# Optimization experiments

Measured on AMD Instinct MI355X. Metric: run time of the kernel, lower is better.

Reference implementation:

```python
import jax, jax.numpy as jnp
import numpy as np

N_NODES = 10000
N_EDGES = 160000
IN_FEAT = 1024
H_FEAT = 1024
NUM_CLASSES = 64


def setup_inputs() -> dict:
    key = jax.random.key(0)
    ks = jax.random.split(key, 8)
    h = jax.random.normal(ks[0], (N_NODES, IN_FEAT), dtype=jnp.float32)
    src = jax.random.randint(ks[1], (N_EDGES,), 0, N_NODES, dtype=jnp.int32)
    dst = jax.random.randint(ks[2], (N_EDGES,), 0, N_NODES, dtype=jnp.int32)
    # Xavier-ish scaled weights (DGL uses xavier_uniform for GraphConv)
    W1 = jax.random.normal(ks[3], (IN_FEAT, H_FEAT), dtype=jnp.float32) * (1.0 / np.sqrt(IN_FEAT))
    b1 = jnp.zeros((H_FEAT,), dtype=jnp.float32)
    W2 = jax.random.normal(ks[4], (H_FEAT, H_FEAT), dtype=jnp.float32) * (1.0 / np.sqrt(H_FEAT))
    b2 = jnp.zeros((H_FEAT,), dtype=jnp.float32)
    W3 = jax.random.normal(ks[5], (H_FEAT, NUM_CLASSES), dtype=jnp.float32) * (1.0 / np.sqrt(H_FEAT))
    b3 = jnp.zeros((NUM_CLASSES,), dtype=jnp.float32)
    return {"h": h, "src": src, "dst": dst,
            "W1": W1, "b1": b1, "W2": W2, "b2": b2, "W3": W3, "b3": b3}


def _graph_conv(src, dst, norm_src, norm_dst, x, W, b):
    """DGL GraphConv with norm='both':
    out = D_dst^{-1/2} * sum_{(u,v) in E} (D_src^{-1/2} * x)_u  @ W + b
    """
    xs = x * norm_src[:, None]                     # [N, d] scaled source feats
    msg = xs[src]                                  # [E, d] gather
    agg = jax.ops.segment_sum(msg, dst, num_segments=N_NODES)  # [N, d] scatter-add
    agg = agg * norm_dst[:, None]
    return agg @ W + b


def reference(h, src, dst, W1, b1, W2, b2, W3, b3):
    ones = jnp.ones((N_EDGES,), dtype=jnp.float32)
    deg_out = jax.ops.segment_sum(ones, src, num_segments=N_NODES)  # out-degree of src
    deg_in = jax.ops.segment_sum(ones, dst, num_segments=N_NODES)   # in-degree of dst
    norm_src = jnp.clip(deg_out, 1.0, None) ** -0.5
    norm_dst = jnp.clip(deg_in, 1.0, None) ** -0.5

    x = _graph_conv(src, dst, norm_src, norm_dst, h, W1, b1)
    x = jax.nn.relu(x)
    x = _graph_conv(src, dst, norm_src, norm_dst, x, W2, b2)
    x = jax.nn.relu(x)
    x = _graph_conv(src, dst, norm_src, norm_dst, x, W3, b3)
    return x
```

## Files before the change

kernel.cpp:

```cpp
#include <hip/hip_runtime.h>

constexpr int NN   = 10000;
constexpr int NE   = 160000;
constexpr int F    = 1024;
constexpr int C3   = 64;
constexpr int MPAD = 10112;

typedef __attribute__((ext_vector_type(8))) short short8;
typedef __attribute__((ext_vector_type(8))) unsigned short ushort8v;
typedef __attribute__((ext_vector_type(4))) float floatx4;

__device__ __forceinline__ unsigned short f2bf(float f) {
    union { float f; unsigned u; } v; v.f = f;
    unsigned r = v.u + 0x7fff + ((v.u >> 16) & 1);
    return (unsigned short)(r >> 16);
}
__device__ __forceinline__ float bf2f(unsigned short u) {
    union { unsigned u; float f; } v; v.u = ((unsigned)u) << 16;
    return v.f;
}

__device__ __forceinline__ void gl_lds16(const void* g, void* l) {
    __builtin_amdgcn_global_load_lds(
        (const __attribute__((address_space(1))) unsigned int*)g,
        (__attribute__((address_space(3))) unsigned int*)l, 16, 0, 0);
}


__global__ __launch_bounds__(256) void k_degree(const int* __restrict__ src,
                                                const int* __restrict__ dst,
                                                int* __restrict__ deg_out,
                                                int* __restrict__ deg_in) {
    int e = blockIdx.x * 256 + threadIdx.x;
    if (e < NE) {
        atomicAdd(&deg_out[src[e]], 1);
        atomicAdd(&deg_in[dst[e]], 1);
    }
}

__global__ __launch_bounds__(1024) void k_scan(const int* __restrict__ deg_in,
                                               const int* __restrict__ deg_out,
                                               int* __restrict__ row_ptr,
                                               int* __restrict__ cursor,
                                               float* __restrict__ norm_src,
                                               float* __restrict__ norm_dst) {
    constexpr int CH = 10;
    __shared__ int sums[1024];
    const int tid = threadIdx.x;
    int local[CH];
    int tsum = 0;
#pragma unroll
    for (int j = 0; j < CH; ++j) {
        int idx = tid * CH + j;
        int v = (idx < NN) ? deg_in[idx] : 0;
        local[j] = v;
        tsum += v;
        if (idx < MPAD) {
            norm_src[idx] = rsqrtf(fmaxf((float)deg_out[idx], 1.0f));
            norm_dst[idx] = rsqrtf(fmaxf((float)deg_in[idx], 1.0f));
        }
    }
    sums[tid] = tsum;
    __syncthreads();
    for (int off = 1; off < 1024; off <<= 1) {
        int v = (tid >= off) ? sums[tid - off] : 0;
        __syncthreads();
        sums[tid] += v;
        __syncthreads();
    }
    int run = sums[tid] - tsum;
#pragma unroll
    for (int j = 0; j < CH; ++j) {
        int idx = tid * CH + j;
        if (idx < NN) {
            row_ptr[idx] = run;
            cursor[idx]  = run;
        }
        run += local[j];
    }
    if (tid == 1023) row_ptr[NN] = sums[1023];
}

__global__ __launch_bounds__(256) void k_bucket(const int* __restrict__ src,
                                                const int* __restrict__ dst,
                                                int* __restrict__ cursor,
                                                int* __restrict__ csr_src) {
    int e = blockIdx.x * 256 + threadIdx.x;
    if (e < NE) {
        int slot = atomicAdd(&cursor[dst[e]], 1);
        csr_src[slot] = src[e];
    }
}

__global__ __launch_bounds__(256) void k_wconv_all(const float* __restrict__ W1,
                                                   const float* __restrict__ W2,
                                                   const float* __restrict__ W3,
                                                   unsigned short* __restrict__ Wt1,
                                                   unsigned short* __restrict__ Wt2,
                                                   unsigned short* __restrict__ Wt3) {
    __shared__ float tile[32][33];
    const float* W; unsigned short* Wt; int N, n0, k0;
    int b = blockIdx.x;
    if (b < 1024)      { W = W1; Wt = Wt1; N = F;  n0 = (b & 31) * 32;          k0 = (b >> 5) * 32; }
    else if (b < 2048) { b -= 1024; W = W2; Wt = Wt2; N = F;  n0 = (b & 31) * 32; k0 = (b >> 5) * 32; }
    else               { b -= 2048; W = W3; Wt = Wt3; N = C3; n0 = (b & 1) * 32;  k0 = (b >> 1) * 32; }
    const int tx = threadIdx.x & 31, ty = threadIdx.x >> 5;
#pragma unroll
    for (int i = 0; i < 32; i += 8)
        tile[ty + i][tx] = W[(size_t)(k0 + ty + i) * N + n0 + tx];
    __syncthreads();
#pragma unroll
    for (int i = 0; i < 32; i += 8)
        Wt[(size_t)(n0 + ty + i) * F + k0 + tx] = f2bf(tile[tx][ty + i]);
}


__global__ __launch_bounds__(256) void k_hcvt(const float* __restrict__ h,
                                              const float* __restrict__ norm_src,
                                              unsigned short* __restrict__ hb) {
    int idx = blockIdx.x * 256 + threadIdx.x;
    int v = idx >> 7, f8 = (idx & 127) * 8;
    float ns = norm_src[v];
    const float4 a = *(const float4*)(h + (size_t)v * F + f8);
    const float4 b = *(const float4*)(h + (size_t)v * F + f8 + 4);
    ushort8v o;
    o[0] = f2bf(ns * a.x); o[1] = f2bf(ns * a.y);
    o[2] = f2bf(ns * a.z); o[3] = f2bf(ns * a.w);
    o[4] = f2bf(ns * b.x); o[5] = f2bf(ns * b.y);
    o[6] = f2bf(ns * b.z); o[7] = f2bf(ns * b.w);
    *(ushort8v*)(hb + (size_t)v * F + f8) = o;
}

__global__ __launch_bounds__(256) void k_aggb(const unsigned short* __restrict__ xb,
                                              const int* __restrict__ row_ptr,
                                              const int* __restrict__ csr_src,
                                              unsigned short* __restrict__ aggb) {
    const int c = blockIdx.x & 7;
    const int g = blockIdx.x >> 3;
    const int v = g * 16 + (threadIdx.x >> 4);
    const int f8 = c * 128 + (threadIdx.x & 15) * 8;
    const int lo = row_ptr[v], hi = row_ptr[v + 1];
    float acc[8] = {0.f, 0.f, 0.f, 0.f, 0.f, 0.f, 0.f, 0.f};
    int i = lo;
    for (; i + 4 <= hi; i += 4) {
        int s0 = csr_src[i],     s1 = csr_src[i + 1];
        int s2 = csr_src[i + 2], s3 = csr_src[i + 3];
        ushort8v x0 = *(const ushort8v*)(xb + (size_t)s0 * F + f8);
        ushort8v x1 = *(const ushort8v*)(xb + (size_t)s1 * F + f8);
        ushort8v x2 = *(const ushort8v*)(xb + (size_t)s2 * F + f8);
        ushort8v x3 = *(const ushort8v*)(xb + (size_t)s3 * F + f8);
#pragma unroll
        for (int j = 0; j < 8; ++j) acc[j] += bf2f(x0[j]);
#pragma unroll
        for (int j = 0; j < 8; ++j) acc[j] += bf2f(x1[j]);
#pragma unroll
        for (int j = 0; j < 8; ++j) acc[j] += bf2f(x2[j]);
#pragma unroll
        for (int j = 0; j < 8; ++j) acc[j] += bf2f(x3[j]);
    }
    for (; i < hi; ++i) {
        int s = csr_src[i];
        ushort8v xv = *(const ushort8v*)(xb + (size_t)s * F + f8);
#pragma unroll
        for (int j = 0; j < 8; ++j) acc[j] += bf2f(xv[j]);
    }
    ushort8v o;
#pragma unroll
    for (int j = 0; j < 8; ++j) o[j] = f2bf(acc[j]);
    *(ushort8v*)(aggb + (size_t)v * F + f8) = o;
}

__global__ __launch_bounds__(256) void k_agg64(const float* __restrict__ z,
                                               const int* __restrict__ row_ptr,
                                               const int* __restrict__ csr_src,
                                               const float* __restrict__ norm_dst,
                                               const float* __restrict__ b3,
                                               float* __restrict__ out) {
    const int v = blockIdx.x * 16 + (threadIdx.x >> 4);
    if (v >= NN) return;
    const int f4 = (threadIdx.x & 15) * 4;
    const int lo = row_ptr[v], hi = row_ptr[v + 1];
    float4 acc = {0.f, 0.f, 0.f, 0.f};
    int i = lo;
    for (; i + 2 <= hi; i += 2) {
        int s0 = csr_src[i], s1 = csr_src[i + 1];
        float4 z0 = *(const float4*)(z + (size_t)s0 * C3 + f4);
        float4 z1 = *(const float4*)(z + (size_t)s1 * C3 + f4);
        acc.x += z0.x; acc.y += z0.y; acc.z += z0.z; acc.w += z0.w;
        acc.x += z1.x; acc.y += z1.y; acc.z += z1.z; acc.w += z1.w;
    }
    if (i < hi) {
        int s = csr_src[i];
        float4 zv = *(const float4*)(z + (size_t)s * C3 + f4);
        acc.x += zv.x; acc.y += zv.y; acc.z += zv.z; acc.w += zv.w;
    }
    float nd = norm_dst[v];
    float4 bv = *(const float4*)(b3 + f4);
    float4 o;
    o.x = acc.x * nd + bv.x; o.y = acc.y * nd + bv.y;
    o.z = acc.z * nd + bv.z; o.w = acc.w * nd + bv.w;
    *(float4*)(out + (size_t)v * C3 + f4) = o;
}

__global__ __launch_bounds__(512) void k_gemm_bf16(
        const unsigned short* __restrict__ A,
        const unsigned short* __restrict__ Bt,
        const float* __restrict__ bias,
        const float* __restrict__ rs1,
        const float* __restrict__ rs2,
        unsigned short* __restrict__ Cb) {
    __shared__ short As[2][128 * 32];
    __shared__ short Bs[2][128 * 32];
    const int t = threadIdx.x, lane = t & 63, wid = t >> 6;
    const int m0 = blockIdx.x * 128, n0 = blockIdx.y * 128;
    const int wm0 = (wid & 1) * 64, wn0 = (wid >> 1) * 32;
    const int lr = lane & 15, q = lane >> 4;

    const int rS  = wid * 16 + (lane >> 2);
    const int sS  = (((lane & 3) ^ ((rS >> 1) & 3)) * 8);
    const unsigned short* aSrc = A  + (size_t)(m0 + rS) * F + sS;
    const unsigned short* bSrc = Bt + (size_t)(n0 + rS) * F + sS;
    short* aDst = &As[0][wid * 512];
    short* bDst = &Bs[0][wid * 512];

    const short* ap[4];
    const short* bp[2];
#pragma unroll
    for (int mb = 0; mb < 4; ++mb) {
        int m = wm0 + mb * 16 + lr;
        ap[mb] = &As[0][m * 32 + (q ^ ((m >> 1) & 3)) * 8];
    }
#pragma unroll
    for (int nb = 0; nb < 2; ++nb) {
        int n = wn0 + nb * 16 + lr;
        bp[nb] = &Bs[0][n * 32 + (q ^ ((n >> 1) & 3)) * 8];
    }

    floatx4 acc[4][2] = {};

    gl_lds16(aSrc, aDst);
    gl_lds16(bSrc, bDst);

    for (int kt = 0; kt < F / 32; ++kt) {
        const int buf = kt & 1;
        __syncthreads();
        if (kt + 1 < F / 32) {
            int k0 = (kt + 1) * 32;
            gl_lds16(aSrc + k0, aDst + (buf ^ 1) * (128 * 32));
            gl_lds16(bSrc + k0, bDst + (buf ^ 1) * (128 * 32));
        }
        const int bo = buf * (128 * 32);
        short8 af[4], bf[2];
#pragma unroll
        for (int mb = 0; mb < 4; ++mb) af[mb] = *(const short8*)(ap[mb] + bo);
#pragma unroll
        for (int nb = 0; nb < 2; ++nb) bf[nb] = *(const short8*)(bp[nb] + bo);
#pragma unroll
        for (int mb = 0; mb < 4; ++mb)
#pragma unroll
            for (int nb = 0; nb < 2; ++nb)
                acc[mb][nb] = __builtin_amdgcn_mfma_f32_16x16x32_bf16(
                    af[mb], bf[nb], acc[mb][nb], 0, 0, 0);
    }

    float s1[4][4], s2[4][4];
#pragma unroll
    for (int mb = 0; mb < 4; ++mb)
#pragma unroll
        for (int r = 0; r < 4; ++r) {
            int row = m0 + wm0 + mb * 16 + q * 4 + r;
            s1[mb][r] = rs1[row];
            s2[mb][r] = rs2[row];
        }
#pragma unroll
    for (int nb = 0; nb < 2; ++nb) {
        int col = n0 + wn0 + nb * 16 + lr;
        float bv = bias[col];
#pragma unroll
        for (int mb = 0; mb < 4; ++mb)
#pragma unroll
            for (int r = 0; r < 4; ++r) {
                int row = m0 + wm0 + mb * 16 + q * 4 + r;
                float v = fmaxf(acc[mb][nb][r] * s1[mb][r] + bv, 0.f) * s2[mb][r];
                Cb[(size_t)row * F + col] = f2bf(v);
            }
    }
}

__global__ __launch_bounds__(256) void k_gemm3(
        const unsigned short* __restrict__ A,
        const unsigned short* __restrict__ Bt,
        float* __restrict__ Z) {
    __shared__ short As3[2][64 * 32];
    __shared__ short Bs3[2][64 * 32];
    const int t = threadIdx.x, lane = t & 63, wid = t >> 6;
    const int m0 = blockIdx.x * 64;
    const int lr = lane & 15, q = lane >> 4;

    const int r = wid * 16 + (lane >> 2);
    const int soff = (((lane & 3) ^ ((r >> 1) & 3)) * 8);
    const unsigned short* aSrc = A  + (size_t)(m0 + r) * F + soff;
    const unsigned short* bSrc = Bt + (size_t)r * F + soff;

    const short* ap;
    {
        int m = wid * 16 + lr;
        ap = &As3[0][m * 32 + (q ^ ((m >> 1) & 3)) * 8];
    }
    const short* bp[4];
#pragma unroll
    for (int nb = 0; nb < 4; ++nb) {
        int n = nb * 16 + lr;
        bp[nb] = &Bs3[0][n * 32 + (q ^ ((n >> 1) & 3)) * 8];
    }

    floatx4 acc[4] = {};

    gl_lds16(aSrc, &As3[0][wid * 512]);
    gl_lds16(bSrc, &Bs3[0][wid * 512]);

    for (int kt = 0; kt < F / 32; ++kt) {
        const int buf = kt & 1;
        __syncthreads();
        if (kt + 1 < F / 32) {
            int k0 = (kt + 1) * 32;
            gl_lds16(aSrc + k0, &As3[buf ^ 1][wid * 512]);
            gl_lds16(bSrc + k0, &Bs3[buf ^ 1][wid * 512]);
        }
        const int bo = buf * (64 * 32);
        short8 af = *(const short8*)(ap + bo);
        short8 bf[4];
#pragma unroll
        for (int nb = 0; nb < 4; ++nb) bf[nb] = *(const short8*)(bp[nb] + bo);
#pragma unroll
        for (int nb = 0; nb < 4; ++nb)
            acc[nb] = __builtin_amdgcn_mfma_f32_16x16x32_bf16(af, bf[nb], acc[nb], 0, 0, 0);
    }

#pragma unroll
    for (int nb = 0; nb < 4; ++nb) {
        int col = nb * 16 + lr;
#pragma unroll
        for (int ri = 0; ri < 4; ++ri) {
            int row = m0 + wid * 16 + q * 4 + ri;
            Z[(size_t)row * C3 + col] = acc[nb][ri];
        }
    }
}


extern "C" void kernel_launch(void* const* d_in, const int* in_sizes, int n_in,
                              void* d_out, int out_size, void* d_ws, size_t ws_size,
                              hipStream_t stream) {
    const float* h   = (const float*)d_in[0];
    const int*   src = (const int*)d_in[1];
    const int*   dst = (const int*)d_in[2];
    const float* W1  = (const float*)d_in[3];
    const float* b1  = (const float*)d_in[4];
    const float* W2  = (const float*)d_in[5];
    const float* b2  = (const float*)d_in[6];
    const float* W3  = (const float*)d_in[7];
    const float* b3  = (const float*)d_in[8];
    float* out = (float*)d_out;

    char* ws = (char*)d_ws;
    int*   deg_out  = (int*)ws;                       ws += MPAD * 4;
    int*   deg_in   = (int*)ws;                       ws += MPAD * 4;
    float* norm_src = (float*)ws;                     ws += MPAD * 4;
    float* norm_dst = (float*)ws;                     ws += MPAD * 4;
    int*   row_ptr  = (int*)ws;                       ws += (NN + 1) * 4;
    int*   cursor   = (int*)ws;                       ws += NN * 4;
    int*   csr_src  = (int*)ws;                       ws += NE * 4;
    ws = (char*)(((size_t)ws + 255) & ~(size_t)255);
    unsigned short* hb   = (unsigned short*)ws;       ws += (size_t)MPAD * F * 2;
    unsigned short* aggb = (unsigned short*)ws;       ws += (size_t)MPAD * F * 2;
    unsigned short* xb   = (unsigned short*)ws;       ws += (size_t)MPAD * F * 2;
    unsigned short* Wt1  = (unsigned short*)ws;       ws += (size_t)F * F * 2;
    unsigned short* Wt2  = (unsigned short*)ws;       ws += (size_t)F * F * 2;
    unsigned short* Wt3  = (unsigned short*)ws;       ws += (size_t)C3 * F * 2;
    float* z3       = (float*)ws;

    hipMemsetAsync(deg_out, 0, 2 * MPAD * sizeof(int), stream);
    k_degree<<<(NE + 255) / 256, 256, 0, stream>>>(src, dst, deg_out, deg_in);
    k_scan<<<1, 1024, 0, stream>>>(deg_in, deg_out, row_ptr, cursor, norm_src, norm_dst);
    k_bucket<<<(NE + 255) / 256, 256, 0, stream>>>(src, dst, cursor, csr_src);
    k_wconv_all<<<2112, 256, 0, stream>>>(W1, W2, W3, Wt1, Wt2, Wt3);
    k_hcvt<<<NN * 128 / 256, 256, 0, stream>>>(h, norm_src, hb);

    k_aggb<<<(NN / 16) * 8, 256, 0, stream>>>(hb, row_ptr, csr_src, aggb);
    k_gemm_bf16<<<dim3(MPAD / 128, F / 128), 512, 0, stream>>>(aggb, Wt1, b1, norm_dst, norm_src, xb);

    k_aggb<<<(NN / 16) * 8, 256, 0, stream>>>(xb, row_ptr, csr_src, aggb);
    k_gemm_bf16<<<dim3(MPAD / 128, F / 128), 512, 0, stream>>>(aggb, Wt2, b2, norm_dst, norm_src, xb);

    k_gemm3<<<MPAD / 64, 256, 0, stream>>>(xb, Wt3, z3);
    k_agg64<<<(NN + 15) / 16, 256, 0, stream>>>(z3, row_ptr, csr_src, norm_dst, b3, out);
}
```

Before: 296.8 us.

## Remap GEMM blocks for XCD-aware locality and deepen gather unrolling

The GEMM launch becomes a 1D grid. Block indices are remapped so that consecutive blocks, which round-robin across the 8 XCDs, land on the same chiplet in contiguous M-row groups sharing A tiles, and MPAD is padded to 10240 (80 row tiles) to make the mapping even. The aggregation kernels unroll the neighbor gather from 4 to 8 (bf16) and from 2 to 4 (fp32) to keep more loads in flight per thread. The risks are higher register pressure in the gather kernels and extra padded rows in the GEMM.

```diff
diff --git a/kernel.cpp b/kernel.cpp
--- a/kernel.cpp
+++ b/kernel.cpp
@@ -4,7 +4,7 @@
 constexpr int NE   = 160000;
 constexpr int F    = 1024;
 constexpr int C3   = 64;
-constexpr int MPAD = 10112;
+constexpr int MPAD = 10240;
 
 typedef __attribute__((ext_vector_type(8))) short short8;
 typedef __attribute__((ext_vector_type(8))) unsigned short ushort8v;
@@ -139,16 +139,23 @@
     const int g = blockIdx.x >> 3;
     const int v = g * 16 + (threadIdx.x >> 4);
     const int f8 = c * 128 + (threadIdx.x & 15) * 8;
+    const unsigned short* xr = xb + f8;
     const int lo = row_ptr[v], hi = row_ptr[v + 1];
     float acc[8] = {0.f, 0.f, 0.f, 0.f, 0.f, 0.f, 0.f, 0.f};
     int i = lo;
-    for (; i + 4 <= hi; i += 4) {
+    for (; i + 8 <= hi; i += 8) {
         int s0 = csr_src[i],     s1 = csr_src[i + 1];
         int s2 = csr_src[i + 2], s3 = csr_src[i + 3];
-        ushort8v x0 = *(const ushort8v*)(xb + (size_t)s0 * F + f8);
-        ushort8v x1 = *(const ushort8v*)(xb + (size_t)s1 * F + f8);
-        ushort8v x2 = *(const ushort8v*)(xb + (size_t)s2 * F + f8);
-        ushort8v x3 = *(const ushort8v*)(xb + (size_t)s3 * F + f8);
+        int s4 = csr_src[i + 4], s5 = csr_src[i + 5];
+        int s6 = csr_src[i + 6], s7 = csr_src[i + 7];
+        ushort8v x0 = *(const ushort8v*)(xr + (size_t)s0 * F);
+        ushort8v x1 = *(const ushort8v*)(xr + (size_t)s1 * F);
+        ushort8v x2 = *(const ushort8v*)(xr + (size_t)s2 * F);
+        ushort8v x3 = *(const ushort8v*)(xr + (size_t)s3 * F);
+        ushort8v x4 = *(const ushort8v*)(xr + (size_t)s4 * F);
+        ushort8v x5 = *(const ushort8v*)(xr + (size_t)s5 * F);
+        ushort8v x6 = *(const ushort8v*)(xr + (size_t)s6 * F);
+        ushort8v x7 = *(const ushort8v*)(xr + (size_t)s7 * F);
 #pragma unroll
         for (int j = 0; j < 8; ++j) acc[j] += bf2f(x0[j]);
 #pragma unroll
@@ -157,10 +164,35 @@
         for (int j = 0; j < 8; ++j) acc[j] += bf2f(x2[j]);
 #pragma unroll
         for (int j = 0; j < 8; ++j) acc[j] += bf2f(x3[j]);
+#pragma unroll
+        for (int j = 0; j < 8; ++j) acc[j] += bf2f(x4[j]);
+#pragma unroll
+        for (int j = 0; j < 8; ++j) acc[j] += bf2f(x5[j]);
+#pragma unroll
+        for (int j = 0; j < 8; ++j) acc[j] += bf2f(x6[j]);
+#pragma unroll
+        for (int j = 0; j < 8; ++j) acc[j] += bf2f(x7[j]);
+    }
+    if (i + 4 <= hi) {
+        int s0 = csr_src[i],     s1 = csr_src[i + 1];
+        int s2 = csr_src[i + 2], s3 = csr_src[i + 3];
+        ushort8v x0 = *(const ushort8v*)(xr + (size_t)s0 * F);
+        ushort8v x1 = *(const ushort8v*)(xr + (size_t)s1 * F);
+        ushort8v x2 = *(const ushort8v*)(xr + (size_t)s2 * F);
+        ushort8v x3 = *(const ushort8v*)(xr + (size_t)s3 * F);
+#pragma unroll
+        for (int j = 0; j < 8; ++j) acc[j] += bf2f(x0[j]);
+#pragma unroll
+        for (int j = 0; j < 8; ++j) acc[j] += bf2f(x1[j]);
+#pragma unroll
+        for (int j = 0; j < 8; ++j) acc[j] += bf2f(x2[j]);
+#pragma unroll
+        for (int j = 0; j < 8; ++j) acc[j] += bf2f(x3[j]);
+        i += 4;
     }
     for (; i < hi; ++i) {
         int s = csr_src[i];
-        ushort8v xv = *(const ushort8v*)(xb + (size_t)s * F + f8);
+        ushort8v xv = *(const ushort8v*)(xr + (size_t)s * F);
 #pragma unroll
         for (int j = 0; j < 8; ++j) acc[j] += bf2f(xv[j]);
     }
@@ -182,14 +214,19 @@
     const int lo = row_ptr[v], hi = row_ptr[v + 1];
     float4 acc = {0.f, 0.f, 0.f, 0.f};
     int i = lo;
-    for (; i + 2 <= hi; i += 2) {
-        int s0 = csr_src[i], s1 = csr_src[i + 1];
+    for (; i + 4 <= hi; i += 4) {
+        int s0 = csr_src[i],     s1 = csr_src[i + 1];
+        int s2 = csr_src[i + 2], s3 = csr_src[i + 3];
         float4 z0 = *(const float4*)(z + (size_t)s0 * C3 + f4);
         float4 z1 = *(const float4*)(z + (size_t)s1 * C3 + f4);
-        acc.x += z0.x; acc.y += z0.y; acc.z += z0.z; acc.w += z0.w;
-        acc.x += z1.x; acc.y += z1.y; acc.z += z1.z; acc.w += z1.w;
-    }
-    if (i < hi) {
+        float4 z2 = *(const float4*)(z + (size_t)s2 * C3 + f4);
+        float4 z3v = *(const float4*)(z + (size_t)s3 * C3 + f4);
+        acc.x += z0.x + z1.x + z2.x + z3v.x;
+        acc.y += z0.y + z1.y + z2.y + z3v.y;
+        acc.z += z0.z + z1.z + z2.z + z3v.z;
+        acc.w += z0.w + z1.w + z2.w + z3v.w;
+    }
+    for (; i < hi; ++i) {
         int s = csr_src[i];
         float4 zv = *(const float4*)(z + (size_t)s * C3 + f4);
         acc.x += zv.x; acc.y += zv.y; acc.z += zv.z; acc.w += zv.w;
@@ -212,7 +249,9 @@
     __shared__ short As[2][128 * 32];
     __shared__ short Bs[2][128 * 32];
     const int t = threadIdx.x, lane = t & 63, wid = t >> 6;
-    const int m0 = blockIdx.x * 128, n0 = blockIdx.y * 128;
+    const int j = blockIdx.x >> 3;
+    const int m0 = ((blockIdx.x & 7) * 10 + (j >> 3)) * 128;
+    const int n0 = (j & 7) * 128;
     const int wm0 = (wid & 1) * 64, wn0 = (wid >> 1) * 32;
     const int lr = lane & 15, q = lane >> 4;
 
@@ -388,10 +427,10 @@
     k_hcvt<<<NN * 128 / 256, 256, 0, stream>>>(h, norm_src, hb);
 
     k_aggb<<<(NN / 16) * 8, 256, 0, stream>>>(hb, row_ptr, csr_src, aggb);
-    k_gemm_bf16<<<dim3(MPAD / 128, F / 128), 512, 0, stream>>>(aggb, Wt1, b1, norm_dst, norm_src, xb);
+    k_gemm_bf16<<<(MPAD / 128) * (F / 128), 512, 0, stream>>>(aggb, Wt1, b1, norm_dst, norm_src, xb);
 
     k_aggb<<<(NN / 16) * 8, 256, 0, stream>>>(xb, row_ptr, csr_src, aggb);
-    k_gemm_bf16<<<dim3(MPAD / 128, F / 128), 512, 0, stream>>>(aggb, Wt2, b2, norm_dst, norm_src, xb);
+    k_gemm_bf16<<<(MPAD / 128) * (F / 128), 512, 0, stream>>>(aggb, Wt2, b2, norm_dst, norm_src, xb);
 
     k_gemm3<<<MPAD / 64, 256, 0, stream>>>(xb, Wt3, z3);
     k_agg64<<<(NN + 15) / 16, 256, 0, stream>>>(z3, row_ptr, csr_src, norm_dst, b3, out);
```

Measured after the change: 277.7 us. -6.4%, faster.

## Pad CSR rows to multiples of eight and remap GEMM tile order

Applied to the files above, without the earlier changes.

Each node's CSR segment is padded up to a multiple of eight, with the padding pointing at a dummy all-zero row (index MPAD) in hb, xb and z3. The aggregation kernels can then load indices as int4 and gather eight (or four) rows per iteration with no scalar tail loop. The GEMM grid is flattened, and tile indices are remapped so that consecutive blocks cover a group of M tiles across all N tiles, aiming for better L2 reuse. MPAD grows to 10240, which adds padded GEMM work. Initialising the enlarged CSR buffer inside the single-block scan kernel is extra serial work.

```diff
diff --git a/kernel.cpp b/kernel.cpp
--- a/kernel.cpp
+++ b/kernel.cpp
@@ -4,7 +4,8 @@
 constexpr int NE   = 160000;
 constexpr int F    = 1024;
 constexpr int C3   = 64;
-constexpr int MPAD = 10112;
+constexpr int MPAD = 10240;
+constexpr int CSRCAP = NE + NN * 8;
 
 typedef __attribute__((ext_vector_type(8))) short short8;
 typedef __attribute__((ext_vector_type(8))) unsigned short ushort8v;
@@ -43,21 +44,24 @@
                                                int* __restrict__ row_ptr,
                                                int* __restrict__ cursor,
                                                float* __restrict__ norm_src,
-                                               float* __restrict__ norm_dst) {
+                                               float* __restrict__ norm_dst,
+                                               int* __restrict__ csr_src) {
     constexpr int CH = 10;
     __shared__ int sums[1024];
     const int tid = threadIdx.x;
+    for (int i = tid; i < CSRCAP; i += 1024) csr_src[i] = MPAD;
     int local[CH];
     int tsum = 0;
 #pragma unroll
     for (int j = 0; j < CH; ++j) {
         int idx = tid * CH + j;
-        int v = (idx < NN) ? deg_in[idx] : 0;
-        local[j] = v;
-        tsum += v;
+        int d = (idx < NN) ? deg_in[idx] : 0;
+        int pd = (idx < NN) ? ((d + 7) & ~7) : 0;
+        local[j] = pd;
+        tsum += pd;
         if (idx < MPAD) {
             norm_src[idx] = rsqrtf(fmaxf((float)deg_out[idx], 1.0f));
-            norm_dst[idx] = rsqrtf(fmaxf((float)deg_in[idx], 1.0f));
+            norm_dst[idx] = rsqrtf(fmaxf((float)d, 1.0f));
         }
     }
     sums[tid] = tsum;
@@ -117,9 +121,17 @@
 
 __global__ __launch_bounds__(256) void k_hcvt(const float* __restrict__ h,
                                               const float* __restrict__ norm_src,
-                                              unsigned short* __restrict__ hb) {
+                                              unsigned short* __restrict__ hb,
+                                              unsigned short* __restrict__ xb) {
     int idx = blockIdx.x * 256 + threadIdx.x;
+    if (idx >= (MPAD + 1) * 128) return;
     int v = idx >> 7, f8 = (idx & 127) * 8;
+    if (v >= NN) {
+        ushort8v z = {0, 0, 0, 0, 0, 0, 0, 0};
+        *(ushort8v*)(hb + (size_t)v * F + f8) = z;
+        *(ushort8v*)(xb + (size_t)v * F + f8) = z;
+        return;
+    }
     float ns = norm_src[v];
     const float4 a = *(const float4*)(h + (size_t)v * F + f8);
     const float4 b = *(const float4*)(h + (size_t)v * F + f8 + 4);
@@ -139,16 +151,20 @@
     const int g = blockIdx.x >> 3;
     const int v = g * 16 + (threadIdx.x >> 4);
     const int f8 = c * 128 + (threadIdx.x & 15) * 8;
+    const unsigned short* xr = xb + f8;
     const int lo = row_ptr[v], hi = row_ptr[v + 1];
     float acc[8] = {0.f, 0.f, 0.f, 0.f, 0.f, 0.f, 0.f, 0.f};
-    int i = lo;
-    for (; i + 4 <= hi; i += 4) {
-        int s0 = csr_src[i],     s1 = csr_src[i + 1];
-        int s2 = csr_src[i + 2], s3 = csr_src[i + 3];
-        ushort8v x0 = *(const ushort8v*)(xb + (size_t)s0 * F + f8);
-        ushort8v x1 = *(const ushort8v*)(xb + (size_t)s1 * F + f8);
-        ushort8v x2 = *(const ushort8v*)(xb + (size_t)s2 * F + f8);
-        ushort8v x3 = *(const ushort8v*)(xb + (size_t)s3 * F + f8);
+    for (int i = lo; i < hi; i += 8) {
+        const int4 ia = *(const int4*)(csr_src + i);
+        const int4 ib = *(const int4*)(csr_src + i + 4);
+        ushort8v x0 = *(const ushort8v*)(xr + (size_t)ia.x * F);
+        ushort8v x1 = *(const ushort8v*)(xr + (size_t)ia.y * F);
+        ushort8v x2 = *(const ushort8v*)(xr + (size_t)ia.z * F);
+        ushort8v x3 = *(const ushort8v*)(xr + (size_t)ia.w * F);
+        ushort8v x4 = *(const ushort8v*)(xr + (size_t)ib.x * F);
+        ushort8v x5 = *(const ushort8v*)(xr + (size_t)ib.y * F);
+        ushort8v x6 = *(const ushort8v*)(xr + (size_t)ib.z * F);
+        ushort8v x7 = *(const ushort8v*)(xr + (size_t)ib.w * F);
 #pragma unroll
         for (int j = 0; j < 8; ++j) acc[j] += bf2f(x0[j]);
 #pragma unroll
@@ -157,12 +173,14 @@
         for (int j = 0; j < 8; ++j) acc[j] += bf2f(x2[j]);
 #pragma unroll
         for (int j = 0; j < 8; ++j) acc[j] += bf2f(x3[j]);
-    }
-    for (; i < hi; ++i) {
-        int s = csr_src[i];
-        ushort8v xv = *(const ushort8v*)(xb + (size_t)s * F + f8);
-#pragma unroll
-        for (int j = 0; j < 8; ++j) acc[j] += bf2f(xv[j]);
+#pragma unroll
+        for (int j = 0; j < 8; ++j) acc[j] += bf2f(x4[j]);
+#pragma unroll
+        for (int j = 0; j < 8; ++j) acc[j] += bf2f(x5[j]);
+#pragma unroll
+        for (int j = 0; j < 8; ++j) acc[j] += bf2f(x6[j]);
+#pragma unroll
+        for (int j = 0; j < 8; ++j) acc[j] += bf2f(x7[j]);
     }
     ushort8v o;
 #pragma unroll
@@ -181,18 +199,16 @@
     const int f4 = (threadIdx.x & 15) * 4;
     const int lo = row_ptr[v], hi = row_ptr[v + 1];
     float4 acc = {0.f, 0.f, 0.f, 0.f};
-    int i = lo;
-    for (; i + 2 <= hi; i += 2) {
-        int s0 = csr_src[i], s1 = csr_src[i + 1];
-        float4 z0 = *(const float4*)(z + (size_t)s0 * C3 + f4);
-        float4 z1 = *(const float4*)(z + (size_t)s1 * C3 + f4);
-        acc.x += z0.x; acc.y += z0.y; acc.z += z0.z; acc.w += z0.w;
-        acc.x += z1.x; acc.y += z1.y; acc.z += z1.z; acc.w += z1.w;
-    }
-    if (i < hi) {
-        int s = csr_src[i];
-        float4 zv = *(const float4*)(z + (size_t)s * C3 + f4);
-        acc.x += zv.x; acc.y += zv.y; acc.z += zv.z; acc.w += zv.w;
+    for (int i = lo; i + 4 <= hi; i += 4) {
+        const int4 s = *(const int4*)(csr_src + i);
+        float4 z0 = *(const float4*)(z + (size_t)s.x * C3 + f4);
+        float4 z1 = *(const float4*)(z + (size_t)s.y * C3 + f4);
+        float4 z2 = *(const float4*)(z + (size_t)s.z * C3 + f4);
+        float4 z3v = *(const float4*)(z + (size_t)s.w * C3 + f4);
+        acc.x += z0.x + z1.x + z2.x + z3v.x;
+        acc.y += z0.y + z1.y + z2.y + z3v.y;
+        acc.z += z0.z + z1.z + z2.z + z3v.z;
+        acc.w += z0.w + z1.w + z2.w + z3v.w;
     }
     float nd = norm_dst[v];
     float4 bv = *(const float4*)(b3 + f4);
@@ -212,7 +228,9 @@
     __shared__ short As[2][128 * 32];
     __shared__ short Bs[2][128 * 32];
     const int t = threadIdx.x, lane = t & 63, wid = t >> 6;
-    const int m0 = blockIdx.x * 128, n0 = blockIdx.y * 128;
+    const int j = blockIdx.x >> 3;
+    const int m0 = ((blockIdx.x & 7) * 10 + (j >> 3)) * 128;
+    const int n0 = (j & 7) * 128;
     const int wm0 = (wid & 1) * 64, wn0 = (wid >> 1) * 32;
     const int lr = lane & 15, q = lane >> 4;
 
@@ -370,28 +388,29 @@
     float* norm_dst = (float*)ws;                     ws += MPAD * 4;
     int*   row_ptr  = (int*)ws;                       ws += (NN + 1) * 4;
     int*   cursor   = (int*)ws;                       ws += NN * 4;
-    int*   csr_src  = (int*)ws;                       ws += NE * 4;
+    int*   csr_src  = (int*)ws;                       ws += CSRCAP * 4;
     ws = (char*)(((size_t)ws + 255) & ~(size_t)255);
-    unsigned short* hb   = (unsigned short*)ws;       ws += (size_t)MPAD * F * 2;
+    unsigned short* hb   = (unsigned short*)ws;       ws += (size_t)(MPAD + 1) * F * 2;
     unsigned short* aggb = (unsigned short*)ws;       ws += (size_t)MPAD * F * 2;
-    unsigned short* xb   = (unsigned short*)ws;       ws += (size_t)MPAD * F * 2;
+    unsigned short* xb   = (unsigned short*)ws;       ws += (size_t)(MPAD + 1) * F * 2;
     unsigned short* Wt1  = (unsigned short*)ws;       ws += (size_t)F * F * 2;
     unsigned short* Wt2  = (unsigned short*)ws;       ws += (size_t)F * F * 2;
     unsigned short* Wt3  = (unsigned short*)ws;       ws += (size_t)C3 * F * 2;
     float* z3       = (float*)ws;
 
     hipMemsetAsync(deg_out, 0, 2 * MPAD * sizeof(int), stream);
+    hipMemsetAsync(z3 + (size_t)MPAD * C3, 0, C3 * sizeof(float), stream);
     k_degree<<<(NE + 255) / 256, 256, 0, stream>>>(src, dst, deg_out, deg_in);
-    k_scan<<<1, 1024, 0, stream>>>(deg_in, deg_out, row_ptr, cursor, norm_src, norm_dst);
+    k_scan<<<1, 1024, 0, stream>>>(deg_in, deg_out, row_ptr, cursor, norm_src, norm_dst, csr_src);
     k_bucket<<<(NE + 255) / 256, 256, 0, stream>>>(src, dst, cursor, csr_src);
     k_wconv_all<<<2112, 256, 0, stream>>>(W1, W2, W3, Wt1, Wt2, Wt3);
-    k_hcvt<<<NN * 128 / 256, 256, 0, stream>>>(h, norm_src, hb);
+    k_hcvt<<<((MPAD + 1) * 128 + 255) / 256, 256, 0, stream>>>(h, norm_src, hb, xb);
 
     k_aggb<<<(NN / 16) * 8, 256, 0, stream>>>(hb, row_ptr, csr_src, aggb);
-    k_gemm_bf16<<<dim3(MPAD / 128, F / 128), 512, 0, stream>>>(aggb, Wt1, b1, norm_dst, norm_src, xb);
+    k_gemm_bf16<<<(MPAD / 128) * (F / 128), 512, 0, stream>>>(aggb, Wt1, b1, norm_dst, norm_src, xb);
 
     k_aggb<<<(NN / 16) * 8, 256, 0, stream>>>(xb, row_ptr, csr_src, aggb);
-    k_gemm_bf16<<<dim3(MPAD / 128, F / 128), 512, 0, stream>>>(aggb, Wt2, b2, norm_dst, norm_src, xb);
+    k_gemm_bf16<<<(MPAD / 128) * (F / 128), 512, 0, stream>>>(aggb, Wt2, b2, norm_dst, norm_src, xb);
 
     k_gemm3<<<MPAD / 64, 256, 0, stream>>>(xb, Wt3, z3);
     k_agg64<<<(NN + 15) / 16, 256, 0, stream>>>(z3, row_ptr, csr_src, norm_dst, b3, out);
```

Result: no change. 291.3 us (-1.9%).
